# Kernel tuning notes

Measured on AMD Instinct MI355X. Metric: run time of the kernel, lower is better.

The kernel has to match this reference:

```python
import jax, jax.numpy as jnp
from jax import lax
import numpy as np

N_LOOP, N_LAYER, FS = 2, 10, 2
RES_CH, DIL_CH, SKIP_CH, COND_DIM = 64, 128, 128, 80
DILATIONS = [2 ** i for i in range(N_LAYER)] * N_LOOP  # 20 layers
L = len(DILATIONS)
B, T = 4, 8192


def setup_inputs() -> dict:
    key = jax.random.key(0)
    ks = jax.random.split(key, 10)
    s = 0.05
    return {
        "x": jax.random.normal(ks[0], (B, RES_CH, T, 1), jnp.float32),
        "condition": jax.random.normal(ks[1], (B, COND_DIM, T, 1), jnp.float32),
        # stacked per-layer params (L layers)
        "conv_w": jax.random.normal(ks[2], (L, DIL_CH, RES_CH, FS), jnp.float32) * s,
        "conv_b": jax.random.normal(ks[3], (L, DIL_CH), jnp.float32) * s,
        "cond_w": jax.random.normal(ks[4], (L, DIL_CH, COND_DIM), jnp.float32) * s,
        "cond_b": jax.random.normal(ks[5], (L, DIL_CH), jnp.float32) * s,
        "res_w": jax.random.normal(ks[6], (L, RES_CH, DIL_CH // 2), jnp.float32) * s,
        "res_b": jax.random.normal(ks[7], (L, RES_CH), jnp.float32) * s,
        "skip_w": jax.random.normal(ks[8], (L, SKIP_CH, DIL_CH // 2), jnp.float32) * s,
        "skip_b": jax.random.normal(ks[9], (L, SKIP_CH), jnp.float32) * s,
    }


def reference(x, condition, conv_w, conv_b, cond_w, cond_b, res_w, res_b, skip_w, skip_b):
    # Drop trailing width-1 dim: [B,C,T,1] -> [B,C,T]
    xs = x[..., 0]
    cond = condition[..., 0]
    skip_total = None
    for i, d in enumerate(DILATIONS):
        # torch pads d*(FS-1) on both sides then crops [:T] == left-only causal pad
        h = lax.conv_general_dilated(
            xs, conv_w[i], window_strides=(1,),
            padding=[(d * (FS - 1), 0)], rhs_dilation=(d,),
            dimension_numbers=("NCH", "OIH", "NCH"),
        ) + conv_b[i][None, :, None]
        # 1x1 condition projection, broadcast add
        h = h + jnp.einsum("ch,bht->bct", cond_w[i], cond) + cond_b[i][None, :, None]
        tanh_z, sig_z = jnp.split(h, 2, axis=1)
        z = jnp.tanh(tanh_z) * jax.nn.sigmoid(sig_z)  # [B, DIL_CH//2, T]
        xs = jnp.einsum("oc,bct->bot", res_w[i], z) + res_b[i][None, :, None] + xs
        skip = jnp.einsum("oc,bct->bot", skip_w[i], z) + skip_b[i][None, :, None]
        skip_total = skip if skip_total is None else skip_total + skip
    return skip_total[..., None]  # [B, SKIP_CH, T, 1]
```

## Files before the change

### kernel.cpp

```cpp
#include <hip/hip_runtime.h>

#define BATCH 4
#define TLEN 8192
#define NLAYER 20
#define NTILE 128
#define GUARD 8
#define ATILE (NTILE + GUARD)
#define CELL 4096

typedef __attribute__((ext_vector_type(8))) short bf16x8;
typedef __attribute__((ext_vector_type(8))) unsigned short u16x8;
typedef __attribute__((ext_vector_type(4))) short s16x4;
typedef __attribute__((ext_vector_type(4))) float f32x4;

__device__ __forceinline__ unsigned short f2b(float f) {
    unsigned u = __float_as_uint(f);
    return (unsigned short)((u + 0x7fffu + ((u >> 16) & 1u)) >> 16);
}

__device__ __forceinline__ unsigned cvtpk(float lo, float hi) {
    unsigned r;
    asm("v_cvt_pk_bf16_f32 %0, %1, %2" : "=v"(r) : "v"(lo), "v"(hi));
    return r;
}

__global__ void prep_w(const float* __restrict__ conv_w, const float* __restrict__ conv_b,
                       const float* __restrict__ cond_w, const float* __restrict__ cond_b,
                       const float* __restrict__ res_w,  const float* __restrict__ res_b,
                       const float* __restrict__ skip_w, const float* __restrict__ skip_b,
                       unsigned short* __restrict__ w1f, unsigned short* __restrict__ w2f,
                       unsigned short* __restrict__ wsf,
                       float* __restrict__ hb, float* __restrict__ rb, float* __restrict__ sbt) {
    const int l = blockIdx.x, tid = threadIdx.x;
    const int start = blockIdx.y * 256 + tid;
    for (int idx = start; idx < 7 * 8 * 512; idx += 2048) {
        int ks = idx >> 12;
        int slot = (idx >> 9) & 7, lane = (idx >> 3) & 63, j = idx & 7;
        int m = (slot & 1) * 64 + (slot >> 1) * 16 + (lane & 15);
        int k = ks * 32 + ((lane >> 4) << 3) + j;
        float v;
        if (k < 64)       v = conv_w[(((size_t)l * 128 + m) * 64 + k) * 2 + 0];
        else if (k < 128) v = conv_w[(((size_t)l * 128 + m) * 64 + (k - 64)) * 2 + 1];
        else if (k < 208) v = cond_w[((size_t)l * 128 + m) * 80 + (k - 128)];
        else              v = 0.0f;
        w1f[(size_t)l * 7 * 8 * 512 + idx] = f2b(v);
    }
    for (int idx = start; idx < 2 * 4 * 512; idx += 2048) {
        int ks = idx >> 11;
        int slot = (idx >> 9) & 3, lane = (idx >> 3) & 63, j = idx & 7;
        int m = slot * 16 + (lane & 15);
        int k = ks * 32 + ((lane >> 4) << 3) + j;
        w2f[(size_t)l * 2 * 4 * 512 + idx] = f2b(res_w[((size_t)l * 64 + m) * 64 + k]);
    }
    for (int idx = start; idx < 2 * 8 * 512; idx += 2048) {
        int ks = idx >> 12;
        int slot = (idx >> 9) & 7, lane = (idx >> 3) & 63, j = idx & 7;
        int m = slot * 16 + (lane & 15);
        int k = ks * 32 + ((lane >> 4) << 3) + j;
        wsf[(size_t)l * 2 * 8 * 512 + idx] = f2b(skip_w[((size_t)l * 128 + m) * 64 + k]);
    }
    if (blockIdx.y == 0) {
        if (tid < 128) hb[l * 128 + tid] = conv_b[l * 128 + tid] + cond_b[l * 128 + tid];
        if (tid < 64)  rb[l * 64 + tid] = res_b[l * 64 + tid];
        if (l == 0 && tid < 128) {
            float s = 0.f;
            for (int q = 0; q < NLAYER; ++q) s += skip_b[q * 128 + tid];
            sbt[tid] = s;
        }
    }
}

__global__ void prep_xc(const float* __restrict__ x, const float* __restrict__ cond,
                        unsigned short* __restrict__ xall, unsigned short* __restrict__ condc,
                        unsigned* __restrict__ flags) {
    const int tile = blockIdx.x, b = blockIdx.y, tid = threadIdx.x;
    if (tile < GUARD) {
        s16x4 zh = {0, 0, 0, 0};
        for (int s = 0; s < NLAYER; ++s) {
            unsigned short* g = xall + ((size_t)s * BATCH + b) * ATILE * CELL + (size_t)tile * CELL;
            for (int idx = tid * 4; idx < CELL; idx += 1024)
                *(s16x4*)(g + idx) = zh;
        }
        if (tile == 0)
            for (int i = tid; i < NTILE * 32; i += 256)
                flags[(size_t)b * NTILE * 32 + i] = 0u;
        return;
    }
    __shared__ float xt[64][64];
    __shared__ float ct[80][64];
    const int rt = tile - GUARD;
    for (int idx = tid; idx < 64 * 64; idx += 256) {
        int ch = idx >> 6, n = idx & 63;
        xt[ch][n] = x[((size_t)b * 64 + ch) * TLEN + rt * 64 + n];
    }
    for (int idx = tid; idx < 80 * 64; idx += 256) {
        int ch = idx >> 6, n = idx & 63;
        ct[ch][n] = cond[((size_t)b * 80 + ch) * TLEN + rt * 64 + n];
    }
    __syncthreads();
    unsigned short* s0 = xall + ((size_t)b * ATILE + tile) * CELL;
    for (int idx = tid; idx < 8 * 64; idx += 256) {
        int cg = idx >> 6, n = idx & 63;
        unsigned short* dbf = s0 + ((size_t)cg * 64 + n) * 8;
        #pragma unroll
        for (int j = 0; j < 8; ++j) dbf[j] = f2b(xt[cg * 8 + j][n]);
    }
    for (int idx = tid; idx < 12 * 64; idx += 256) {
        int cg = idx >> 6, n = idx & 63;
        u16x8 cell;
        #pragma unroll
        for (int j = 0; j < 8; ++j) {
            int ch = cg * 8 + j;
            cell[j] = (ch < 80) ? f2b(ct[ch][n]) : (unsigned short)0;
        }
        *(u16x8*)(condc + (((size_t)(b * NTILE + rt) * 12 + cg) * 64 + n) * 8) = cell;
    }
}

__global__ __launch_bounds__(256, 2) void wavenet_fused(
    const float* __restrict__ x, const unsigned short* __restrict__ condc,
    unsigned short* __restrict__ xall,
    const unsigned short* __restrict__ w1f, const unsigned short* __restrict__ w2f,
    const unsigned short* __restrict__ wsf,
    const float* __restrict__ hb, const float* __restrict__ rb,
    const float* __restrict__ sbt, float* __restrict__ out,
    unsigned* __restrict__ flags) {
    __shared__ unsigned short s_cond[12 * 512];
    __shared__ unsigned short s_xc[CELL];
    __shared__ unsigned short s_zc[CELL];

    const int b = blockIdx.y, tile = blockIdx.x, t0 = tile * 64;
    const int tid = threadIdx.x, lane = tid & 63;
    const int wv = __builtin_amdgcn_readfirstlane(tid >> 6);
    const int ln = lane & 15, lg = lane >> 4;
    const int r0 = wv * 16 + lg * 4;
    const int cgz = r0 >> 3, j0z = r0 & 7;
    const size_t bslot = (size_t)BATCH * ATILE * CELL;

    {
        const u16x8* cc = (const u16x8*)(condc + (size_t)(b * NTILE + tile) * 12 * 512);
        u16x8* sc = (u16x8*)s_cond;
        for (int i = tid; i < 768; i += 256) sc[i] = cc[i];
        const u16x8* xc = (const u16x8*)(xall + ((size_t)b * ATILE + tile + GUARD) * CELL);
        u16x8* sx = (u16x8*)s_xc;
        for (int i = tid; i < 512; i += 256) sx[i] = xc[i];
    }

    f32x4 xsr[4];
    #pragma unroll
    for (int nf = 0; nf < 4; ++nf)
        #pragma unroll
        for (int r = 0; r < 4; ++r)
            xsr[nf][r] = x[((size_t)b * 64 + r0 + r) * TLEN + t0 + nf * 16 + ln];

    f32x4 skacc[2][4];
    #pragma unroll
    for (int mf = 0; mf < 2; ++mf)
        #pragma unroll
        for (int nf = 0; nf < 4; ++nf) skacc[mf][nf] = (f32x4){0.f, 0.f, 0.f, 0.f};

    unsigned fc1 = 0, fc2 = 0, fc4 = 0, fc8 = 0;
    unsigned* myflag = flags + ((size_t)b * NTILE + tile) * 32 + wv;

    __syncthreads();

    for (int l = 0; l < NLAYER; ++l) {
        const int dil = 1 << ((l < 10) ? l : (l - 10));

        if (l > 0) {
            __syncthreads();
            const int kd = (dil + 63) >> 6;
            const int tp = tile - kd;
            if (tp >= 0) {
                unsigned cached = (kd == 1) ? fc1 : (kd == 2) ? fc2 : (kd == 4) ? fc4 : fc8;
                if (cached < (unsigned)l) {
                    const unsigned* fp = flags + ((size_t)b * NTILE + tp) * 32 + (lane & 3);
                    unsigned v;
                    for (;;) {
                        v = __hip_atomic_load(fp, __ATOMIC_RELAXED, __HIP_MEMORY_SCOPE_AGENT);
                        unsigned v1 = (unsigned)__shfl_xor((int)v, 1);
                        v = (v1 < v) ? v1 : v;
                        unsigned v2 = (unsigned)__shfl_xor((int)v, 2);
                        v = (v2 < v) ? v2 : v;
                        if (v >= (unsigned)l) break;
                        __builtin_amdgcn_s_sleep(2);
                    }
                    if (kd == 1) fc1 = v; else if (kd == 2) fc2 = v;
                    else if (kd == 4) fc4 = v; else fc8 = v;
                }
            }
        }

        const unsigned short* xrb = xall + (size_t)l * bslot + (size_t)b * ATILE * CELL;

        f32x4 acc[2][4];
        #pragma unroll
        for (int hf = 0; hf < 2; ++hf)
            #pragma unroll
            for (int nf = 0; nf < 4; ++nf) acc[hf][nf] = (f32x4){0.f, 0.f, 0.f, 0.f};

        const unsigned short* w1l = w1f + (size_t)l * 7 * 8 * 512;
        #pragma unroll
        for (int ks = 0; ks < 7; ++ks) {
            bf16x8 af0 = *(const bf16x8*)(w1l + (size_t)(ks * 8 + wv * 2 + 0) * 512 + lane * 8);
            bf16x8 af1 = *(const bf16x8*)(w1l + (size_t)(ks * 8 + wv * 2 + 1) * 512 + lane * 8);
            bf16x8 bfr[4];
            if (ks < 2) {
                const int cg = ks * 4 + lg;
                #pragma unroll
                for (int nf = 0; nf < 4; ++nf) {
                    int u = t0 + nf * 16 + ln - dil + GUARD * 64;
                    bfr[nf] = *(const bf16x8*)(xrb + (((size_t)(u >> 6) * 8 + cg) * 64 + (u & 63)) * 8);
                }
            } else if (ks < 4) {
                const int cg = (ks - 2) * 4 + lg;
                #pragma unroll
                for (int nf = 0; nf < 4; ++nf)
                    bfr[nf] = *(const bf16x8*)(s_xc + ((cg * 64) + nf * 16 + ln) * 8);
            } else {
                const int cg = (ks - 4) * 4 + lg;
                #pragma unroll
                for (int nf = 0; nf < 4; ++nf)
                    bfr[nf] = *(const bf16x8*)(s_cond + ((cg * 64) + nf * 16 + ln) * 8);
            }
            #pragma unroll
            for (int hf = 0; hf < 2; ++hf)
                #pragma unroll
                for (int nf = 0; nf < 4; ++nf)
                    acc[hf][nf] = __builtin_amdgcn_mfma_f32_16x16x32_bf16(
                        (hf == 0) ? af0 : af1, bfr[nf], acc[hf][nf], 0, 0, 0);
        }

        {
            const float* hbl = hb + l * 128;
            float4 hbt = *(const float4*)(hbl + r0);
            float4 hbs = *(const float4*)(hbl + 64 + r0);
            #pragma unroll
            for (int nf = 0; nf < 4; ++nf) {
                float zr[4];
                #pragma unroll
                for (int r = 0; r < 4; ++r) {
                    float a  = acc[0][nf][r] + ((r == 0) ? hbt.x : (r == 1) ? hbt.y : (r == 2) ? hbt.z : hbt.w);
                    float bs = acc[1][nf][r] + ((r == 0) ? hbs.x : (r == 1) ? hbs.y : (r == 2) ? hbs.z : hbs.w);
                    float e = __expf(a + a);
                    float s = __expf(-bs);
                    zr[r] = __fdividef(e - 1.0f, (e + 1.0f) * (1.0f + s));
                }
                union { unsigned u32[2]; s16x4 v; } pk;
                pk.u32[0] = cvtpk(zr[0], zr[1]);
                pk.u32[1] = cvtpk(zr[2], zr[3]);
                *(s16x4*)(&s_zc[((cgz * 64) + nf * 16 + ln) * 8 + j0z]) = pk.v;
            }
        }
        __syncthreads();

        bf16x8 bz[2][4];
        #pragma unroll
        for (int ks = 0; ks < 2; ++ks)
            #pragma unroll
            for (int nf = 0; nf < 4; ++nf)
                bz[ks][nf] = *(const bf16x8*)(&s_zc[(((ks * 4 + lg) * 64) + nf * 16 + ln) * 8]);

        f32x4 acc2[4];
        #pragma unroll
        for (int nf = 0; nf < 4; ++nf) acc2[nf] = (f32x4){0.f, 0.f, 0.f, 0.f};
        const unsigned short* w2l = w2f + (size_t)l * 2 * 4 * 512;
        #pragma unroll
        for (int ks = 0; ks < 2; ++ks) {
            bf16x8 a2 = *(const bf16x8*)(w2l + (size_t)(ks * 4 + wv) * 512 + lane * 8);
            #pragma unroll
            for (int nf = 0; nf < 4; ++nf)
                acc2[nf] = __builtin_amdgcn_mfma_f32_16x16x32_bf16(a2, bz[ks][nf], acc2[nf], 0, 0, 0);
        }

        {
            const float* rbl = rb + l * 64;
            float4 rbv = *(const float4*)(rbl + r0);
            unsigned short* xwt = xall + (size_t)(l + 1) * bslot +
                                  ((size_t)b * ATILE + tile + GUARD) * CELL;
            #pragma unroll
            for (int nf = 0; nf < 4; ++nf) {
                xsr[nf][0] += acc2[nf][0] + rbv.x;
                xsr[nf][1] += acc2[nf][1] + rbv.y;
                xsr[nf][2] += acc2[nf][2] + rbv.z;
                xsr[nf][3] += acc2[nf][3] + rbv.w;
                if (l < NLAYER - 1) {
                    int n = nf * 16 + ln;
                    union { unsigned u32[2]; s16x4 v; unsigned long long u64; } pk;
                    pk.u32[0] = cvtpk(xsr[nf][0], xsr[nf][1]);
                    pk.u32[1] = cvtpk(xsr[nf][2], xsr[nf][3]);
                    *(s16x4*)(&s_xc[(cgz * 64 + n) * 8 + j0z]) = pk.v;
                    __hip_atomic_store((unsigned long long*)(xwt + ((size_t)cgz * 64 + n) * 8 + j0z),
                                       pk.u64, __ATOMIC_RELAXED, __HIP_MEMORY_SCOPE_AGENT);
                }
            }
        }

        const unsigned short* wsl = wsf + (size_t)l * 2 * 8 * 512;
        #pragma unroll
        for (int ks = 0; ks < 2; ++ks) {
            bf16x8 s0 = *(const bf16x8*)(wsl + (size_t)(ks * 8 + wv * 2 + 0) * 512 + lane * 8);
            bf16x8 s1 = *(const bf16x8*)(wsl + (size_t)(ks * 8 + wv * 2 + 1) * 512 + lane * 8);
            #pragma unroll
            for (int nf = 0; nf < 4; ++nf) {
                skacc[0][nf] = __builtin_amdgcn_mfma_f32_16x16x32_bf16(s0, bz[ks][nf], skacc[0][nf], 0, 0, 0);
                skacc[1][nf] = __builtin_amdgcn_mfma_f32_16x16x32_bf16(s1, bz[ks][nf], skacc[1][nf], 0, 0, 0);
            }
        }

        if (l < NLAYER - 1) {
            asm volatile("s_waitcnt vmcnt(0)" ::: "memory");
            if (lane == 0)
                __hip_atomic_store(myflag, (unsigned)(l + 1),
                                   __ATOMIC_RELAXED, __HIP_MEMORY_SCOPE_AGENT);
        }
    }

    #pragma unroll
    for (int mf = 0; mf < 2; ++mf)
        #pragma unroll
        for (int nf = 0; nf < 4; ++nf)
            #pragma unroll
            for (int r = 0; r < 4; ++r) {
                int m = wv * 32 + mf * 16 + lg * 4 + r;
                out[((size_t)b * 128 + m) * TLEN + t0 + nf * 16 + ln] =
                    skacc[mf][nf][r] + sbt[m];
            }
}

extern "C" void kernel_launch(void* const* d_in, const int* in_sizes, int n_in,
                              void* d_out, int out_size, void* d_ws, size_t ws_size,
                              hipStream_t stream) {
    const float* x      = (const float*)d_in[0];
    const float* cond   = (const float*)d_in[1];
    const float* conv_w = (const float*)d_in[2];
    const float* conv_b = (const float*)d_in[3];
    const float* cond_w = (const float*)d_in[4];
    const float* cond_b = (const float*)d_in[5];
    const float* res_w  = (const float*)d_in[6];
    const float* res_b  = (const float*)d_in[7];
    const float* skip_w = (const float*)d_in[8];
    const float* skip_b = (const float*)d_in[9];
    float* out = (float*)d_out;

    char* ws = (char*)d_ws;
    const size_t XALL  = (size_t)NLAYER * BATCH * ATILE * CELL * 2;
    const size_t COND  = (size_t)BATCH * NTILE * 12 * 512 * 2;
    const size_t W1    = (size_t)NLAYER * 7 * 8 * 512 * 2;
    const size_t W2    = (size_t)NLAYER * 2 * 4 * 512 * 2;
    const size_t WSF   = (size_t)NLAYER * 2 * 8 * 512 * 2;
    const size_t HB    = NLAYER * 128 * 4;
    const size_t RB    = NLAYER * 64 * 4;
    const size_t SBT   = 256 * 4;
    const size_t FLAGS = (size_t)BATCH * NTILE * 32 * 4;

    size_t off = 0;
    unsigned short* xall  = (unsigned short*)(ws + off); off += XALL;
    unsigned short* condc = (unsigned short*)(ws + off); off += COND;
    unsigned short* w1f   = (unsigned short*)(ws + off); off += W1;
    unsigned short* w2f   = (unsigned short*)(ws + off); off += W2;
    unsigned short* wsf   = (unsigned short*)(ws + off); off += WSF;
    float* hb  = (float*)(ws + off); off += HB;
    float* rb  = (float*)(ws + off); off += RB;
    float* sbt = (float*)(ws + off); off += SBT;
    unsigned* flags = (unsigned*)(ws + off); off += FLAGS;

    prep_w<<<dim3(NLAYER, 8), 256, 0, stream>>>(conv_w, conv_b, cond_w, cond_b,
                                                res_w, res_b, skip_w, skip_b,
                                                w1f, w2f, wsf, hb, rb, sbt);
    prep_xc<<<dim3(ATILE, BATCH), 256, 0, stream>>>(x, cond, xall, condc, flags);

    wavenet_fused<<<dim3(NTILE, BATCH), 256, 0, stream>>>(
        x, condc, xall, w1f, w2f, wsf, hb, rb, sbt, out, flags);
}
```

Before: 130.6 us.

## Overlap cross-tile wait with local MFMAs and publish one flag per block

Reorders each layer so the residual-stream and condition MFMAs that use only local shared memory run before spinning on the neighbour tile's flag; the dilated-tap loads from global memory follow the wait. The per-wave flags are merged into a single block flag set after a shared-memory counter reaches four waves, and the flag is published before the skip MFMAs rather than after, so dependent tiles can start sooner. This trades the start-of-layer __syncthreads for one after the residual write and adds an LDS atomic, with a shorter sleep in the poll loop.

```diff
diff --git a/kernel.cpp b/kernel.cpp
--- a/kernel.cpp
+++ b/kernel.cpp
@@ -128,6 +128,7 @@
     __shared__ unsigned short s_cond[12 * 512];
     __shared__ unsigned short s_xc[CELL];
     __shared__ unsigned short s_zc[CELL];
+    __shared__ unsigned s_cnt[NLAYER];
 
     const int b = blockIdx.y, tile = blockIdx.x, t0 = tile * 64;
     const int tid = threadIdx.x, lane = tid & 63;
@@ -145,6 +146,7 @@
         u16x8* sx = (u16x8*)s_xc;
         for (int i = tid; i < 512; i += 256) sx[i] = xc[i];
     }
+    if (tid < NLAYER) s_cnt[tid] = 0u;
 
     f32x4 xsr[4];
     #pragma unroll
@@ -160,38 +162,14 @@
         for (int nf = 0; nf < 4; ++nf) skacc[mf][nf] = (f32x4){0.f, 0.f, 0.f, 0.f};
 
     unsigned fc1 = 0, fc2 = 0, fc4 = 0, fc8 = 0;
-    unsigned* myflag = flags + ((size_t)b * NTILE + tile) * 32 + wv;
+    unsigned* myflag = flags + ((size_t)b * NTILE + tile) * 32;
 
     __syncthreads();
 
     for (int l = 0; l < NLAYER; ++l) {
         const int dil = 1 << ((l < 10) ? l : (l - 10));
-
-        if (l > 0) {
-            __syncthreads();
-            const int kd = (dil + 63) >> 6;
-            const int tp = tile - kd;
-            if (tp >= 0) {
-                unsigned cached = (kd == 1) ? fc1 : (kd == 2) ? fc2 : (kd == 4) ? fc4 : fc8;
-                if (cached < (unsigned)l) {
-                    const unsigned* fp = flags + ((size_t)b * NTILE + tp) * 32 + (lane & 3);
-                    unsigned v;
-                    for (;;) {
-                        v = __hip_atomic_load(fp, __ATOMIC_RELAXED, __HIP_MEMORY_SCOPE_AGENT);
-                        unsigned v1 = (unsigned)__shfl_xor((int)v, 1);
-                        v = (v1 < v) ? v1 : v;
-                        unsigned v2 = (unsigned)__shfl_xor((int)v, 2);
-                        v = (v2 < v) ? v2 : v;
-                        if (v >= (unsigned)l) break;
-                        __builtin_amdgcn_s_sleep(2);
-                    }
-                    if (kd == 1) fc1 = v; else if (kd == 2) fc2 = v;
-                    else if (kd == 4) fc4 = v; else fc8 = v;
-                }
-            }
-        }
-
         const unsigned short* xrb = xall + (size_t)l * bslot + (size_t)b * ATILE * CELL;
+        const unsigned short* w1l = w1f + (size_t)l * 7 * 8 * 512;
 
         f32x4 acc[2][4];
         #pragma unroll
@@ -199,20 +177,18 @@
             #pragma unroll
             for (int nf = 0; nf < 4; ++nf) acc[hf][nf] = (f32x4){0.f, 0.f, 0.f, 0.f};
 
-        const unsigned short* w1l = w1f + (size_t)l * 7 * 8 * 512;
-        #pragma unroll
-        for (int ks = 0; ks < 7; ++ks) {
+        bf16x8 raf[4];
+        raf[0] = *(const bf16x8*)(w1l + (size_t)(0 * 8 + wv * 2 + 0) * 512 + lane * 8);
+        raf[1] = *(const bf16x8*)(w1l + (size_t)(0 * 8 + wv * 2 + 1) * 512 + lane * 8);
+        raf[2] = *(const bf16x8*)(w1l + (size_t)(1 * 8 + wv * 2 + 0) * 512 + lane * 8);
+        raf[3] = *(const bf16x8*)(w1l + (size_t)(1 * 8 + wv * 2 + 1) * 512 + lane * 8);
+
+        #pragma unroll
+        for (int ks = 2; ks < 7; ++ks) {
             bf16x8 af0 = *(const bf16x8*)(w1l + (size_t)(ks * 8 + wv * 2 + 0) * 512 + lane * 8);
             bf16x8 af1 = *(const bf16x8*)(w1l + (size_t)(ks * 8 + wv * 2 + 1) * 512 + lane * 8);
             bf16x8 bfr[4];
-            if (ks < 2) {
-                const int cg = ks * 4 + lg;
-                #pragma unroll
-                for (int nf = 0; nf < 4; ++nf) {
-                    int u = t0 + nf * 16 + ln - dil + GUARD * 64;
-                    bfr[nf] = *(const bf16x8*)(xrb + (((size_t)(u >> 6) * 8 + cg) * 64 + (u & 63)) * 8);
-                }
-            } else if (ks < 4) {
+            if (ks < 4) {
                 const int cg = (ks - 2) * 4 + lg;
                 #pragma unroll
                 for (int nf = 0; nf < 4; ++nf)
@@ -224,11 +200,46 @@
                     bfr[nf] = *(const bf16x8*)(s_cond + ((cg * 64) + nf * 16 + ln) * 8);
             }
             #pragma unroll
-            for (int hf = 0; hf < 2; ++hf)
-                #pragma unroll
-                for (int nf = 0; nf < 4; ++nf)
-                    acc[hf][nf] = __builtin_amdgcn_mfma_f32_16x16x32_bf16(
-                        (hf == 0) ? af0 : af1, bfr[nf], acc[hf][nf], 0, 0, 0);
+            for (int nf = 0; nf < 4; ++nf) {
+                acc[0][nf] = __builtin_amdgcn_mfma_f32_16x16x32_bf16(af0, bfr[nf], acc[0][nf], 0, 0, 0);
+                acc[1][nf] = __builtin_amdgcn_mfma_f32_16x16x32_bf16(af1, bfr[nf], acc[1][nf], 0, 0, 0);
+            }
+        }
+
+        if (l > 0) {
+            const int kd = (dil + 63) >> 6;
+            const int tp = tile - kd;
+            if (tp >= 0) {
+                unsigned cached = (kd == 1) ? fc1 : (kd == 2) ? fc2 : (kd == 4) ? fc4 : fc8;
+                if (cached < (unsigned)l) {
+                    const unsigned* fp = flags + ((size_t)b * NTILE + tp) * 32;
+                    unsigned v;
+                    for (;;) {
+                        v = __hip_atomic_load(fp, __ATOMIC_RELAXED, __HIP_MEMORY_SCOPE_AGENT);
+                        if (v >= (unsigned)l) break;
+                        __builtin_amdgcn_s_sleep(1);
+                    }
+                    if (kd == 1) fc1 = v; else if (kd == 2) fc2 = v;
+                    else if (kd == 4) fc4 = v; else fc8 = v;
+                }
+            }
+        }
+        __builtin_amdgcn_sched_barrier(0);
+
+        #pragma unroll
+        for (int ks = 0; ks < 2; ++ks) {
+            const int cg = ks * 4 + lg;
+            bf16x8 bfr[4];
+            #pragma unroll
+            for (int nf = 0; nf < 4; ++nf) {
+                int u = t0 + nf * 16 + ln - dil + GUARD * 64;
+                bfr[nf] = *(const bf16x8*)(xrb + (((size_t)(u >> 6) * 8 + cg) * 64 + (u & 63)) * 8);
+            }
+            #pragma unroll
+            for (int nf = 0; nf < 4; ++nf) {
+                acc[0][nf] = __builtin_amdgcn_mfma_f32_16x16x32_bf16(raf[ks * 2 + 0], bfr[nf], acc[0][nf], 0, 0, 0);
+                acc[1][nf] = __builtin_amdgcn_mfma_f32_16x16x32_bf16(raf[ks * 2 + 1], bfr[nf], acc[1][nf], 0, 0, 0);
+            }
         }
 
         {
@@ -296,6 +307,17 @@
             }
         }
 
+        if (l < NLAYER - 1) {
+            asm volatile("s_waitcnt vmcnt(0)" ::: "memory");
+            if (lane == 0) {
+                unsigned old = atomicAdd(&s_cnt[l], 1u);
+                if (old == 3u)
+                    __hip_atomic_store(myflag, (unsigned)(l + 1),
+                                       __ATOMIC_RELAXED, __HIP_MEMORY_SCOPE_AGENT);
+            }
+            __syncthreads();
+        }
+
         const unsigned short* wsl = wsf + (size_t)l * 2 * 8 * 512;
         #pragma unroll
         for (int ks = 0; ks < 2; ++ks) {
@@ -306,13 +328,6 @@
                 skacc[0][nf] = __builtin_amdgcn_mfma_f32_16x16x32_bf16(s0, bz[ks][nf], skacc[0][nf], 0, 0, 0);
                 skacc[1][nf] = __builtin_amdgcn_mfma_f32_16x16x32_bf16(s1, bz[ks][nf], skacc[1][nf], 0, 0, 0);
             }
-        }
-
-        if (l < NLAYER - 1) {
-            asm volatile("s_waitcnt vmcnt(0)" ::: "memory");
-            if (lane == 0)
-                __hip_atomic_store(myflag, (unsigned)(l + 1),
-                                   __ATOMIC_RELAXED, __HIP_MEMORY_SCOPE_AGENT);
         }
     }
 
```

Result: slower. 138.1 us (+5.8%).

## Recompute left halo tile locally to skip inter-tile waits for small dilations

Applied to the files above, without the earlier changes.

For layers with dilation below 64, each block now also computes the previous 64-step tile as a halo, held in shared memory, so the causal conv reads come from LDS instead of waiting on the neighbour block's flag. Global publication and flag polling happen only for the layers whose successors need cross-tile data (large dilations and the loop boundary at layer 10, where the halo is reloaded from global). This trades roughly double MFMA work on the early layers, plus more registers and LDS, for fewer global round trips and spin-waits.

```diff
diff --git a/kernel.cpp b/kernel.cpp
--- a/kernel.cpp
+++ b/kernel.cpp
@@ -17,11 +17,13 @@
     unsigned u = __float_as_uint(f);
     return (unsigned short)((u + 0x7fffu + ((u >> 16) & 1u)) >> 16);
 }
-
 __device__ __forceinline__ unsigned cvtpk(float lo, float hi) {
     unsigned r;
     asm("v_cvt_pk_bf16_f32 %0, %1, %2" : "=v"(r) : "v"(lo), "v"(hi));
     return r;
+}
+__device__ __forceinline__ float b2f(unsigned short h) {
+    return __uint_as_float(((unsigned)h) << 16);
 }
 
 __global__ void prep_w(const float* __restrict__ conv_w, const float* __restrict__ conv_b,
@@ -125,9 +127,9 @@
     const float* __restrict__ hb, const float* __restrict__ rb,
     const float* __restrict__ sbt, float* __restrict__ out,
     unsigned* __restrict__ flags) {
-    __shared__ unsigned short s_cond[12 * 512];
-    __shared__ unsigned short s_xc[CELL];
-    __shared__ unsigned short s_zc[CELL];
+    __shared__ unsigned short s_cond[12 * 128 * 8];
+    __shared__ unsigned short s_xc[8 * 128 * 8];
+    __shared__ unsigned short s_zc[8 * 128 * 8];
 
     const int b = blockIdx.y, tile = blockIdx.x, t0 = tile * 64;
     const int tid = threadIdx.x, lane = tid & 63;
@@ -136,22 +138,40 @@
     const int r0 = wv * 16 + lg * 4;
     const int cgz = r0 >> 3, j0z = r0 & 7;
     const size_t bslot = (size_t)BATCH * ATILE * CELL;
+    const float hmask = (tile > 0) ? 1.0f : 0.0f;
 
     {
-        const u16x8* cc = (const u16x8*)(condc + (size_t)(b * NTILE + tile) * 12 * 512);
+        const int ct0 = (tile > 0) ? (tile - 1) : 0;
+        const u16x8* ch = (const u16x8*)(condc + (size_t)(b * NTILE + ct0) * 12 * 512);
+        const u16x8* co = (const u16x8*)(condc + (size_t)(b * NTILE + tile) * 12 * 512);
         u16x8* sc = (u16x8*)s_cond;
-        for (int i = tid; i < 768; i += 256) sc[i] = cc[i];
-        const u16x8* xc = (const u16x8*)(xall + ((size_t)b * ATILE + tile + GUARD) * CELL);
+        for (int i = tid; i < 768; i += 256) {
+            int cg = i >> 6, n = i & 63;
+            sc[cg * 128 + n]      = ch[i];
+            sc[cg * 128 + 64 + n] = co[i];
+        }
+        const u16x8* xh = (const u16x8*)(xall + ((size_t)b * ATILE + tile - 1 + GUARD) * CELL);
+        const u16x8* xo = (const u16x8*)(xall + ((size_t)b * ATILE + tile + GUARD) * CELL);
         u16x8* sx = (u16x8*)s_xc;
-        for (int i = tid; i < 512; i += 256) sx[i] = xc[i];
-    }
-
-    f32x4 xsr[4];
+        for (int i = tid; i < 512; i += 256) {
+            int cg = i >> 6, n = i & 63;
+            sx[cg * 128 + n]      = xh[i];
+            sx[cg * 128 + 64 + n] = xo[i];
+        }
+    }
+
+    f32x4 xsr[4], xsh[4];
     #pragma unroll
-    for (int nf = 0; nf < 4; ++nf)
+    for (int nf = 0; nf < 4; ++nf) {
+        int c = nf * 16 + ln;
         #pragma unroll
         for (int r = 0; r < 4; ++r)
-            xsr[nf][r] = x[((size_t)b * 64 + r0 + r) * TLEN + t0 + nf * 16 + ln];
+            xsr[nf][r] = x[((size_t)b * 64 + r0 + r) * TLEN + t0 + c];
+        int th = t0 - 64 + c;
+        #pragma unroll
+        for (int r = 0; r < 4; ++r)
+            xsh[nf][r] = (th >= 0) ? x[((size_t)b * 64 + r0 + r) * TLEN + th] : 0.0f;
+    }
 
     f32x4 skacc[2][4];
     #pragma unroll
@@ -165,11 +185,16 @@
     __syncthreads();
 
     for (int l = 0; l < NLAYER; ++l) {
-        const int dil = 1 << ((l < 10) ? l : (l - 10));
-
-        if (l > 0) {
-            __syncthreads();
-            const int kd = (dil + 63) >> 6;
+        const int dl = (l < 10) ? l : (l - 10);
+        const int dil = 1 << dl;
+        const bool wide  = (dl < 6);
+        const bool wpub  = (l >= 5 && l <= 9) || (l >= 15 && l <= 18);
+        const bool wwait = (l >= 6 && l <= 10) || (l >= 16);
+
+        if (l > 0) __syncthreads();
+
+        if (wwait) {
+            const int kd = (l == 10) ? 1 : (dil >> 6);
             const int tp = tile - kd;
             if (tp >= 0) {
                 unsigned cached = (kd == 1) ? fc1 : (kd == 2) ? fc2 : (kd == 4) ? fc4 : fc8;
@@ -189,54 +214,69 @@
                     else if (kd == 4) fc4 = v; else fc8 = v;
                 }
             }
-        }
-
-        const unsigned short* xrb = xall + (size_t)l * bslot + (size_t)b * ATILE * CELL;
-
-        f32x4 acc[2][4];
-        #pragma unroll
-        for (int hf = 0; hf < 2; ++hf)
-            #pragma unroll
-            for (int nf = 0; nf < 4; ++nf) acc[hf][nf] = (f32x4){0.f, 0.f, 0.f, 0.f};
+            __builtin_amdgcn_sched_barrier(0);
+        }
+
+        if (l == 10) {
+            const unsigned short* src = xall + (size_t)10 * bslot +
+                                        ((size_t)b * ATILE + tile - 1 + GUARD) * CELL;
+            const u16x8* s8 = (const u16x8*)src;
+            u16x8* sx = (u16x8*)s_xc;
+            for (int i = tid; i < 512; i += 256) {
+                int cg = i >> 6, n = i & 63;
+                sx[cg * 128 + n] = s8[i];
+            }
+            #pragma unroll
+            for (int nf = 0; nf < 4; ++nf) {
+                int c = nf * 16 + ln;
+                s16x4 pk = *(const s16x4*)(src + ((size_t)cgz * 64 + c) * 8 + j0z);
+                xsh[nf][0] = b2f((unsigned short)pk.x);
+                xsh[nf][1] = b2f((unsigned short)pk.y);
+                xsh[nf][2] = b2f((unsigned short)pk.z);
+                xsh[nf][3] = b2f((unsigned short)pk.w);
+            }
+            __syncthreads();
+        }
 
         const unsigned short* w1l = w1f + (size_t)l * 7 * 8 * 512;
-        #pragma unroll
-        for (int ks = 0; ks < 7; ++ks) {
-            bf16x8 af0 = *(const bf16x8*)(w1l + (size_t)(ks * 8 + wv * 2 + 0) * 512 + lane * 8);
-            bf16x8 af1 = *(const bf16x8*)(w1l + (size_t)(ks * 8 + wv * 2 + 1) * 512 + lane * 8);
-            bf16x8 bfr[4];
-            if (ks < 2) {
-                const int cg = ks * 4 + lg;
-                #pragma unroll
-                for (int nf = 0; nf < 4; ++nf) {
-                    int u = t0 + nf * 16 + ln - dil + GUARD * 64;
-                    bfr[nf] = *(const bf16x8*)(xrb + (((size_t)(u >> 6) * 8 + cg) * 64 + (u & 63)) * 8);
-                }
-            } else if (ks < 4) {
-                const int cg = (ks - 2) * 4 + lg;
-                #pragma unroll
-                for (int nf = 0; nf < 4; ++nf)
-                    bfr[nf] = *(const bf16x8*)(s_xc + ((cg * 64) + nf * 16 + ln) * 8);
-            } else {
-                const int cg = (ks - 4) * 4 + lg;
-                #pragma unroll
-                for (int nf = 0; nf < 4; ++nf)
-                    bfr[nf] = *(const bf16x8*)(s_cond + ((cg * 64) + nf * 16 + ln) * 8);
-            }
+        const unsigned short* w2l = w2f + (size_t)l * 2 * 4 * 512;
+        const unsigned short* wsl = wsf + (size_t)l * 2 * 8 * 512;
+        const float* hbl = hb + l * 128;
+        float4 hbt = *(const float4*)(hbl + r0);
+        float4 hbs = *(const float4*)(hbl + 64 + r0);
+        float4 rbv = *(const float4*)(rb + l * 64 + r0);
+        unsigned short* xwt = xall + (size_t)(l + 1) * bslot +
+                              ((size_t)b * ATILE + tile + GUARD) * CELL;
+
+        if (wide) {
+            f32x4 acc[2][8];
             #pragma unroll
             for (int hf = 0; hf < 2; ++hf)
                 #pragma unroll
-                for (int nf = 0; nf < 4; ++nf)
-                    acc[hf][nf] = __builtin_amdgcn_mfma_f32_16x16x32_bf16(
-                        (hf == 0) ? af0 : af1, bfr[nf], acc[hf][nf], 0, 0, 0);
-        }
-
-        {
-            const float* hbl = hb + l * 128;
-            float4 hbt = *(const float4*)(hbl + r0);
-            float4 hbs = *(const float4*)(hbl + 64 + r0);
-            #pragma unroll
-            for (int nf = 0; nf < 4; ++nf) {
+                for (int nf = 0; nf < 8; ++nf) acc[hf][nf] = (f32x4){0.f, 0.f, 0.f, 0.f};
+
+            #pragma unroll
+            for (int ks = 0; ks < 7; ++ks) {
+                bf16x8 af0 = *(const bf16x8*)(w1l + (size_t)(ks * 8 + wv * 2 + 0) * 512 + lane * 8);
+                bf16x8 af1 = *(const bf16x8*)(w1l + (size_t)(ks * 8 + wv * 2 + 1) * 512 + lane * 8);
+                #pragma unroll
+                for (int nf = 0; nf < 8; ++nf) {
+                    int n = nf * 16 + ln;
+                    bf16x8 bfr;
+                    if (ks < 2) {
+                        int nt = n - dil; nt = (nt < 0) ? 0 : nt;
+                        bfr = *(const bf16x8*)(s_xc + (((ks * 4 + lg) * 128 + nt) * 8));
+                    } else if (ks < 4) {
+                        bfr = *(const bf16x8*)(s_xc + ((((ks - 2) * 4 + lg) * 128 + n) * 8));
+                    } else {
+                        bfr = *(const bf16x8*)(s_cond + ((((ks - 4) * 4 + lg) * 128 + n) * 8));
+                    }
+                    acc[0][nf] = __builtin_amdgcn_mfma_f32_16x16x32_bf16(af0, bfr, acc[0][nf], 0, 0, 0);
+                    acc[1][nf] = __builtin_amdgcn_mfma_f32_16x16x32_bf16(af1, bfr, acc[1][nf], 0, 0, 0);
+                }
+            }
+            #pragma unroll
+            for (int nf = 0; nf < 8; ++nf) {
                 float zr[4];
                 #pragma unroll
                 for (int r = 0; r < 4; ++r) {
@@ -249,70 +289,166 @@
                 union { unsigned u32[2]; s16x4 v; } pk;
                 pk.u32[0] = cvtpk(zr[0], zr[1]);
                 pk.u32[1] = cvtpk(zr[2], zr[3]);
-                *(s16x4*)(&s_zc[((cgz * 64) + nf * 16 + ln) * 8 + j0z]) = pk.v;
-            }
-        }
-        __syncthreads();
-
-        bf16x8 bz[2][4];
-        #pragma unroll
-        for (int ks = 0; ks < 2; ++ks)
-            #pragma unroll
-            for (int nf = 0; nf < 4; ++nf)
-                bz[ks][nf] = *(const bf16x8*)(&s_zc[(((ks * 4 + lg) * 64) + nf * 16 + ln) * 8]);
-
-        f32x4 acc2[4];
-        #pragma unroll
-        for (int nf = 0; nf < 4; ++nf) acc2[nf] = (f32x4){0.f, 0.f, 0.f, 0.f};
-        const unsigned short* w2l = w2f + (size_t)l * 2 * 4 * 512;
-        #pragma unroll
-        for (int ks = 0; ks < 2; ++ks) {
-            bf16x8 a2 = *(const bf16x8*)(w2l + (size_t)(ks * 4 + wv) * 512 + lane * 8);
-            #pragma unroll
-            for (int nf = 0; nf < 4; ++nf)
-                acc2[nf] = __builtin_amdgcn_mfma_f32_16x16x32_bf16(a2, bz[ks][nf], acc2[nf], 0, 0, 0);
-        }
-
-        {
-            const float* rbl = rb + l * 64;
-            float4 rbv = *(const float4*)(rbl + r0);
-            unsigned short* xwt = xall + (size_t)(l + 1) * bslot +
-                                  ((size_t)b * ATILE + tile + GUARD) * CELL;
+                *(s16x4*)(&s_zc[((cgz * 128) + nf * 16 + ln) * 8 + j0z]) = pk.v;
+            }
+            __syncthreads();
+
+            f32x4 acc2[8];
+            #pragma unroll
+            for (int nf = 0; nf < 8; ++nf) acc2[nf] = (f32x4){0.f, 0.f, 0.f, 0.f};
+            #pragma unroll
+            for (int ks = 0; ks < 2; ++ks) {
+                bf16x8 a2 = *(const bf16x8*)(w2l + (size_t)(ks * 4 + wv) * 512 + lane * 8);
+                #pragma unroll
+                for (int nf = 0; nf < 8; ++nf) {
+                    bf16x8 bz = *(const bf16x8*)(&s_zc[(((ks * 4 + lg) * 128) + nf * 16 + ln) * 8]);
+                    acc2[nf] = __builtin_amdgcn_mfma_f32_16x16x32_bf16(a2, bz, acc2[nf], 0, 0, 0);
+                }
+            }
             #pragma unroll
             for (int nf = 0; nf < 4; ++nf) {
+                int n = nf * 16 + ln;
+                xsh[nf][0] = (xsh[nf][0] + acc2[nf][0] + rbv.x) * hmask;
+                xsh[nf][1] = (xsh[nf][1] + acc2[nf][1] + rbv.y) * hmask;
+                xsh[nf][2] = (xsh[nf][2] + acc2[nf][2] + rbv.z) * hmask;
+                xsh[nf][3] = (xsh[nf][3] + acc2[nf][3] + rbv.w) * hmask;
+                union { unsigned u32[2]; s16x4 v; } pk;
+                pk.u32[0] = cvtpk(xsh[nf][0], xsh[nf][1]);
+                pk.u32[1] = cvtpk(xsh[nf][2], xsh[nf][3]);
+                *(s16x4*)(&s_xc[(cgz * 128 + n) * 8 + j0z]) = pk.v;
+            }
+            #pragma unroll
+            for (int nf = 4; nf < 8; ++nf) {
+                int f = nf - 4;
+                int n = nf * 16 + ln;
+                xsr[f][0] += acc2[nf][0] + rbv.x;
+                xsr[f][1] += acc2[nf][1] + rbv.y;
+                xsr[f][2] += acc2[nf][2] + rbv.z;
+                xsr[f][3] += acc2[nf][3] + rbv.w;
+                union { unsigned u32[2]; s16x4 v; unsigned long long u64; } pk;
+                pk.u32[0] = cvtpk(xsr[f][0], xsr[f][1]);
+                pk.u32[1] = cvtpk(xsr[f][2], xsr[f][3]);
+                *(s16x4*)(&s_xc[(cgz * 128 + n) * 8 + j0z]) = pk.v;
+                if (wpub)
+                    __hip_atomic_store((unsigned long long*)(xwt + ((size_t)cgz * 64 + (n - 64)) * 8 + j0z),
+                                       pk.u64, __ATOMIC_RELAXED, __HIP_MEMORY_SCOPE_AGENT);
+            }
+            if (wpub) {
+                asm volatile("s_waitcnt vmcnt(0)" ::: "memory");
+                if (lane == 0)
+                    __hip_atomic_store(myflag, (unsigned)(l + 1),
+                                       __ATOMIC_RELAXED, __HIP_MEMORY_SCOPE_AGENT);
+            }
+            #pragma unroll
+            for (int ks = 0; ks < 2; ++ks) {
+                bf16x8 s0 = *(const bf16x8*)(wsl + (size_t)(ks * 8 + wv * 2 + 0) * 512 + lane * 8);
+                bf16x8 s1 = *(const bf16x8*)(wsl + (size_t)(ks * 8 + wv * 2 + 1) * 512 + lane * 8);
+                #pragma unroll
+                for (int nf = 4; nf < 8; ++nf) {
+                    bf16x8 bz = *(const bf16x8*)(&s_zc[(((ks * 4 + lg) * 128) + nf * 16 + ln) * 8]);
+                    skacc[0][nf - 4] = __builtin_amdgcn_mfma_f32_16x16x32_bf16(s0, bz, skacc[0][nf - 4], 0, 0, 0);
+                    skacc[1][nf - 4] = __builtin_amdgcn_mfma_f32_16x16x32_bf16(s1, bz, skacc[1][nf - 4], 0, 0, 0);
+                }
+            }
+        } else {
+            const unsigned short* xrb = xall + (size_t)l * bslot + (size_t)b * ATILE * CELL;
+            f32x4 acc[2][4];
+            #pragma unroll
+            for (int hf = 0; hf < 2; ++hf)
+                #pragma unroll
+                for (int nf = 0; nf < 4; ++nf) acc[hf][nf] = (f32x4){0.f, 0.f, 0.f, 0.f};
+
+            #pragma unroll
+            for (int ks = 0; ks < 7; ++ks) {
+                bf16x8 af0 = *(const bf16x8*)(w1l + (size_t)(ks * 8 + wv * 2 + 0) * 512 + lane * 8);
+                bf16x8 af1 = *(const bf16x8*)(w1l + (size_t)(ks * 8 + wv * 2 + 1) * 512 + lane * 8);
+                bf16x8 bfr[4];
+                if (ks < 2) {
+                    const int cg = ks * 4 + lg;
+                    #pragma unroll
+                    for (int nf = 0; nf < 4; ++nf) {
+                        int u = t0 + nf * 16 + ln - dil + GUARD * 64;
+                        bfr[nf] = *(const bf16x8*)(xrb + (((size_t)(u >> 6) * 8 + cg) * 64 + (u & 63)) * 8);
+                    }
+                } else if (ks < 4) {
+                    const int cg = (ks - 2) * 4 + lg;
+                    #pragma unroll
+                    for (int nf = 0; nf < 4; ++nf)
+                        bfr[nf] = *(const bf16x8*)(s_xc + ((cg * 128 + 64 + nf * 16 + ln) * 8));
+                } else {
+                    const int cg = (ks - 4) * 4 + lg;
+                    #pragma unroll
+                    for (int nf = 0; nf < 4; ++nf)
+                        bfr[nf] = *(const bf16x8*)(s_cond + ((cg * 128 + 64 + nf * 16 + ln) * 8));
+                }
+                #pragma unroll
+                for (int nf = 0; nf < 4; ++nf) {
+                    acc[0][nf] = __builtin_amdgcn_mfma_f32_16x16x32_bf16(af0, bfr[nf], acc[0][nf], 0, 0, 0);
+                    acc[1][nf] = __builtin_amdgcn_mfma_f32_16x16x32_bf16(af1, bfr[nf], acc[1][nf], 0, 0, 0);
+                }
+            }
+            #pragma unroll
+            for (int nf = 0; nf < 4; ++nf) {
+                float zr[4];
+                #pragma unroll
+                for (int r = 0; r < 4; ++r) {
+                    float a  = acc[0][nf][r] + ((r == 0) ? hbt.x : (r == 1) ? hbt.y : (r == 2) ? hbt.z : hbt.w);
+                    float bs = acc[1][nf][r] + ((r == 0) ? hbs.x : (r == 1) ? hbs.y : (r == 2) ? hbs.z : hbs.w);
+                    float e = __expf(a + a);
+                    float s = __expf(-bs);
+                    zr[r] = __fdividef(e - 1.0f, (e + 1.0f) * (1.0f + s));
+                }
+                union { unsigned u32[2]; s16x4 v; } pk;
+                pk.u32[0] = cvtpk(zr[0], zr[1]);
+                pk.u32[1] = cvtpk(zr[2], zr[3]);
+                *(s16x4*)(&s_zc[((cgz * 128) + 64 + nf * 16 + ln) * 8 + j0z]) = pk.v;
+            }
+            __syncthreads();
+
+            f32x4 acc2[4];
+            #pragma unroll
+            for (int nf = 0; nf < 4; ++nf) acc2[nf] = (f32x4){0.f, 0.f, 0.f, 0.f};
+            #pragma unroll
+            for (int ks = 0; ks < 2; ++ks) {
+                bf16x8 a2 = *(const bf16x8*)(w2l + (size_t)(ks * 4 + wv) * 512 + lane * 8);
+                #pragma unroll
+                for (int nf = 0; nf < 4; ++nf) {
+                    bf16x8 bz = *(const bf16x8*)(&s_zc[(((ks * 4 + lg) * 128) + 64 + nf * 16 + ln) * 8]);
+                    acc2[nf] = __builtin_amdgcn_mfma_f32_16x16x32_bf16(a2, bz, acc2[nf], 0, 0, 0);
+                }
+            }
+            #pragma unroll
+            for (int nf = 0; nf < 4; ++nf) {
+                int c = nf * 16 + ln;
                 xsr[nf][0] += acc2[nf][0] + rbv.x;
                 xsr[nf][1] += acc2[nf][1] + rbv.y;
                 xsr[nf][2] += acc2[nf][2] + rbv.z;
                 xsr[nf][3] += acc2[nf][3] + rbv.w;
-                if (l < NLAYER - 1) {
-                    int n = nf * 16 + ln;
-                    union { unsigned u32[2]; s16x4 v; unsigned long long u64; } pk;
-                    pk.u32[0] = cvtpk(xsr[nf][0], xsr[nf][1]);
-                    pk.u32[1] = cvtpk(xsr[nf][2], xsr[nf][3]);
-                    *(s16x4*)(&s_xc[(cgz * 64 + n) * 8 + j0z]) = pk.v;
-                    __hip_atomic_store((unsigned long long*)(xwt + ((size_t)cgz * 64 + n) * 8 + j0z),
+                union { unsigned u32[2]; s16x4 v; unsigned long long u64; } pk;
+                pk.u32[0] = cvtpk(xsr[nf][0], xsr[nf][1]);
+                pk.u32[1] = cvtpk(xsr[nf][2], xsr[nf][3]);
+                *(s16x4*)(&s_xc[(cgz * 128 + 64 + c) * 8 + j0z]) = pk.v;
+                if (wpub)
+                    __hip_atomic_store((unsigned long long*)(xwt + ((size_t)cgz * 64 + c) * 8 + j0z),
                                        pk.u64, __ATOMIC_RELAXED, __HIP_MEMORY_SCOPE_AGENT);
-                }
-            }
-        }
-
-        const unsigned short* wsl = wsf + (size_t)l * 2 * 8 * 512;
-        #pragma unroll
-        for (int ks = 0; ks < 2; ++ks) {
-            bf16x8 s0 = *(const bf16x8*)(wsl + (size_t)(ks * 8 + wv * 2 + 0) * 512 + lane * 8);
-            bf16x8 s1 = *(const bf16x8*)(wsl + (size_t)(ks * 8 + wv * 2 + 1) * 512 + lane * 8);
-            #pragma unroll
-            for (int nf = 0; nf < 4; ++nf) {
-                skacc[0][nf] = __builtin_amdgcn_mfma_f32_16x16x32_bf16(s0, bz[ks][nf], skacc[0][nf], 0, 0, 0);
-                skacc[1][nf] = __builtin_amdgcn_mfma_f32_16x16x32_bf16(s1, bz[ks][nf], skacc[1][nf], 0, 0, 0);
-            }
-        }
-
-        if (l < NLAYER - 1) {
-            asm volatile("s_waitcnt vmcnt(0)" ::: "memory");
-            if (lane == 0)
-                __hip_atomic_store(myflag, (unsigned)(l + 1),
-                                   __ATOMIC_RELAXED, __HIP_MEMORY_SCOPE_AGENT);
+            }
+            if (wpub) {
+                asm volatile("s_waitcnt vmcnt(0)" ::: "memory");
+                if (lane == 0)
+                    __hip_atomic_store(myflag, (unsigned)(l + 1),
+                                       __ATOMIC_RELAXED, __HIP_MEMORY_SCOPE_AGENT);
+            }
+            #pragma unroll
+            for (int ks = 0; ks < 2; ++ks) {
+                bf16x8 s0 = *(const bf16x8*)(wsl + (size_t)(ks * 8 + wv * 2 + 0) * 512 + lane * 8);
+                bf16x8 s1 = *(const bf16x8*)(wsl + (size_t)(ks * 8 + wv * 2 + 1) * 512 + lane * 8);
+                #pragma unroll
+                for (int nf = 0; nf < 4; ++nf) {
+                    bf16x8 bz = *(const bf16x8*)(&s_zc[(((ks * 4 + lg) * 128) + 64 + nf * 16 + ln) * 8]);
+                    skacc[0][nf] = __builtin_amdgcn_mfma_f32_16x16x32_bf16(s0, bz, skacc[0][nf], 0, 0, 0);
+                    skacc[1][nf] = __builtin_amdgcn_mfma_f32_16x16x32_bf16(s1, bz, skacc[1][nf], 0, 0, 0);
+                }
+            }
         }
     }
 
```

Result: slower. 158.0 us (+21.0%).
